# Kernel tuning notes

Hardware: AMD Instinct MI355X
Metric: run time of the kernel (lower is better)

Reference implementation:

```python
import jax, jax.numpy as jnp
import numpy as np

H = 1024      # hidden_dim
C = 151       # len(obj_classes)
E = 200       # embed_dim (GloVe)
DIN = 2048    # inputs_dim
T = 32        # timesteps
B = 128       # batch size (uniform packed lengths)


def setup_inputs() -> dict:
    key = jax.random.key(0)
    ks = jax.random.split(key, 8)
    sequence_tensor = jax.random.normal(ks[0], (T * B, DIN), dtype=jnp.float32) * 0.1
    labels = jax.random.randint(ks[1], (T * B,), 0, C).astype(jnp.int64)
    embed = jax.random.normal(ks[2], (C + 1, E), dtype=jnp.float32) * 0.1   # obj_embed.weight
    Wi = jax.random.normal(ks[3], (DIN + E, 6 * H), dtype=jnp.float32) * 0.02  # input_linearity
    bi = jnp.zeros((6 * H,), dtype=jnp.float32)
    Ws = jax.random.normal(ks[4], (H, 5 * H), dtype=jnp.float32) * 0.02        # state_linearity
    bs = jnp.zeros((5 * H,), dtype=jnp.float32)
    Wo = jax.random.normal(ks[5], (H, C), dtype=jnp.float32) * 0.02            # out_obj
    bo = jnp.zeros((C,), dtype=jnp.float32)
    return {"sequence_tensor": sequence_tensor, "labels": labels, "embed": embed,
            "Wi": Wi, "bi": bi, "Ws": Ws, "bs": bs, "Wo": Wo, "bo": bo,
            "batch_size": B}


def reference(sequence_tensor, embed, Wi, bi, Ws, bs, Wo, bo, labels, batch_size):
    b = int(batch_size)
    t = sequence_tensor.shape[0] // b
    x = sequence_tensor.reshape(t, b, -1)          # [T, B, DIN] packed timestep-major
    lab = labels.reshape(t, b)                     # [T, B]
    h0 = jnp.zeros((b, H), dtype=sequence_tensor.dtype)
    c0 = jnp.zeros((b, H), dtype=sequence_tensor.dtype)
    e0 = jnp.broadcast_to(embed[0], (b, E))        # 'start' embedding

    def step(carry, inp):
        h, c, pe = carry
        xt, lt = inp
        ti = jnp.concatenate([xt, pe], axis=1)     # [B, DIN+E]
        pi = ti @ Wi + bi                          # [B, 6H]
        ps = h @ Ws + bs                           # [B, 5H]

        def gate(k):
            return pi[:, k * H:(k + 1) * H] + ps[:, k * H:(k + 1) * H]

        i_g = jax.nn.sigmoid(gate(0))
        f_g = jax.nn.sigmoid(gate(1))
        m_i = jnp.tanh(gate(2))
        o_g = jax.nn.sigmoid(gate(3))
        c_new = i_g * m_i + f_g * c
        out = o_g * jnp.tanh(c_new)
        hw = jax.nn.sigmoid(gate(4))
        h_new = hw * out + (1.0 - hw) * pi[:, 5 * H:6 * H]  # highway

        pred = h_new @ Wo + bo                     # [B, C]
        nzp = jnp.argmax(pred[:, 1:], axis=1) + 1  # best non-bg class
        l2e = jnp.where(lt == 0, nzp.astype(lt.dtype), lt)
        pe_new = embed[l2e + 1]                    # feedback embedding
        return (h_new, c_new, pe_new), (pred, l2e)

    _, (dists, comms) = jax.lax.scan(step, (h0, c0, e0), (x, lab))
    return dists.reshape(t * b, C), comms.reshape(t * b)
```

## Files before the change

kernel.cpp:

```cpp
#include <hip/hip_runtime.h>
#include <math.h>

#define H    1024
#define C    151
#define E    200
#define DIN  2048
#define T    32
#define B    128
#define SIXH  (6*H)
#define FIVEH (5*H)
#define KTOT  DIN
#define NEMB  (C+1)
#define NWG   160
#define COLS  32

typedef _Float16 f16x8 __attribute__((ext_vector_type(8)));
typedef _Float16 f16x4 __attribute__((ext_vector_type(4)));
typedef float    f32x4 __attribute__((ext_vector_type(4)));

#define GLOAD_LDS16(g, l) __builtin_amdgcn_global_load_lds( \
    (const __attribute__((address_space(1))) unsigned int*)(g), \
    (__attribute__((address_space(3))) unsigned int*)(l), 16, 0, 0)

__device__ __forceinline__ void gbar(int* slots, int tid, int val) {
    __syncthreads();
    if (tid == 0)
        __hip_atomic_fetch_add(&slots[blockIdx.x * 16], 1,
                               __ATOMIC_ACQ_REL, __HIP_MEMORY_SCOPE_AGENT);
    int ok;
    do {
        int v = val;
        if (tid < NWG)
            v = __hip_atomic_load(&slots[tid * 16],
                                  __ATOMIC_RELAXED, __HIP_MEMORY_SCOPE_AGENT);
        ok = __syncthreads_and(v >= val);
        if (!ok) __builtin_amdgcn_s_sleep(1);
    } while (!ok);
    __builtin_amdgcn_fence(__ATOMIC_ACQUIRE, "agent");
}

__global__ void init_kernel(float* h, float* c, _Float16* hhi, _Float16* hlo,
                            int* eidx, int* bar) {
    int i = blockIdx.x * blockDim.x + threadIdx.x;
    if (i < B * H) {
        h[i] = 0.f; c[i] = 0.f;
        hhi[i] = (_Float16)0.f; hlo[i] = (_Float16)0.f;
    }
    if (i < B) eidx[i] = 0;
    if (i < NWG * 16) bar[i] = 0;
}

__global__ void cvt_x(const float* __restrict__ X, _Float16* __restrict__ hi,
                      _Float16* __restrict__ lo) {
    size_t i = ((size_t)blockIdx.x * 256 + threadIdx.x) * 4;
    float4 v = *(const float4*)(X + i);
    f16x4 h, l;
    h.x = (_Float16)v.x; l.x = (_Float16)(v.x - (float)h.x);
    h.y = (_Float16)v.y; l.y = (_Float16)(v.y - (float)h.y);
    h.z = (_Float16)v.z; l.z = (_Float16)(v.z - (float)h.z);
    h.w = (_Float16)v.w; l.w = (_Float16)(v.w - (float)h.w);
    *(f16x4*)(hi + i) = h;
    *(f16x4*)(lo + i) = l;
}

template<int KR, int NC>
__global__ void cvt_wT(const float* __restrict__ W, _Float16* __restrict__ hi,
                       _Float16* __restrict__ lo) {
    __shared__ float tile[32][33];
    int n0 = blockIdx.x * 32, k0 = blockIdx.y * 32;
    int tx = threadIdx.x & 31, ty = threadIdx.x >> 5;
    #pragma unroll
    for (int i = 0; i < 4; ++i) {
        int k = ty + i * 8;
        tile[k][tx] = W[(size_t)(k0 + k) * NC + n0 + tx];
    }
    __syncthreads();
    #pragma unroll
    for (int i = 0; i < 4; ++i) {
        int n = ty + i * 8;
        float v = tile[tx][n];
        _Float16 h = (_Float16)v;
        size_t o = (size_t)(n0 + n) * KR + k0 + tx;
        hi[o] = h;
        lo[o] = (_Float16)(v - (float)h);
    }
}

__global__ void cvt_woT(const float* __restrict__ Wo, float* __restrict__ WoT) {
    int k = blockIdx.x * 256 + threadIdx.x;
    for (int c = 0; c < C; ++c)
        WoT[(size_t)c * H + k] = Wo[(size_t)k * C + c];
}

__global__ void etab_kernel(const float* __restrict__ embed,
                            const float* __restrict__ Wi,
                            float* __restrict__ Etab) {
    int n = blockIdx.x * 256 + threadIdx.x;
    int k = blockIdx.y;
    const float* wp = Wi + (size_t)DIN * SIXH + n;
    const float* ep = embed + k * E;
    float acc = 0.f;
    #pragma unroll 8
    for (int e = 0; e < E; ++e)
        acc = fmaf(ep[e], wp[(size_t)e * SIXH], acc);
    Etab[(size_t)k * SIXH + n] = acc;
}

__global__ __launch_bounds__(256) void big_gemm_mfma(
    const _Float16* __restrict__ Ahi, const _Float16* __restrict__ Alo,
    const _Float16* __restrict__ Bhi, const _Float16* __restrict__ Blo,
    const float* __restrict__ bi, float* __restrict__ P)
{
    __shared__ __align__(16) _Float16 sAh[128 * 32];
    __shared__ __align__(16) _Float16 sAl[128 * 32];
    __shared__ __align__(16) _Float16 sBh[128 * 32];
    __shared__ __align__(16) _Float16 sBl[128 * 32];
    const int tid = threadIdx.x;
    const int n0 = blockIdx.x * 128;
    const int m0 = blockIdx.y * 128;
    const int lane = tid & 63, w = tid >> 6;
    const int wm = (w >> 1) * 64, wn = (w & 1) * 64;
    const int lr = lane & 15, lq = lane >> 4;

    f32x4 acc[4][4];
    #pragma unroll
    for (int i = 0; i < 4; ++i)
        #pragma unroll
        for (int j = 0; j < 4; ++j)
            acc[i][j] = (f32x4){0.f, 0.f, 0.f, 0.f};

    const int row0 = tid >> 2;
    const int kc = tid & 3;
    const int kcs = kc ^ ((row0 >> 1) & 3);
    const int sw = (lq ^ ((lr >> 1) & 3)) * 8;

    for (int k0 = 0; k0 < KTOT; k0 += 32) {
        #pragma unroll
        for (int i = 0; i < 2; ++i) {
            int row = row0 + i * 64;
            size_t ga = (size_t)(m0 + row) * KTOT + k0 + kcs * 8;
            size_t gb = (size_t)(n0 + row) * KTOT + k0 + kcs * 8;
            int loff = (i * 256 + tid) * 8;
            GLOAD_LDS16(Ahi + ga, sAh + loff);
            GLOAD_LDS16(Alo + ga, sAl + loff);
            GLOAD_LDS16(Bhi + gb, sBh + loff);
            GLOAD_LDS16(Blo + gb, sBl + loff);
        }
        __syncthreads();
        f16x8 ah[4], al[4], bh[4], bl[4];
        #pragma unroll
        for (int i = 0; i < 4; ++i) {
            ah[i] = *(const f16x8*)&sAh[(wm + i * 16 + lr) * 32 + sw];
            al[i] = *(const f16x8*)&sAl[(wm + i * 16 + lr) * 32 + sw];
            bh[i] = *(const f16x8*)&sBh[(wn + i * 16 + lr) * 32 + sw];
            bl[i] = *(const f16x8*)&sBl[(wn + i * 16 + lr) * 32 + sw];
        }
        #pragma unroll
        for (int i = 0; i < 4; ++i)
            #pragma unroll
            for (int j = 0; j < 4; ++j) {
                acc[i][j] = __builtin_amdgcn_mfma_f32_16x16x32_f16(ah[i], bh[j], acc[i][j], 0, 0, 0);
                acc[i][j] = __builtin_amdgcn_mfma_f32_16x16x32_f16(ah[i], bl[j], acc[i][j], 0, 0, 0);
                acc[i][j] = __builtin_amdgcn_mfma_f32_16x16x32_f16(al[i], bh[j], acc[i][j], 0, 0, 0);
            }
        __syncthreads();
    }
    #pragma unroll
    for (int i = 0; i < 4; ++i)
        #pragma unroll
        for (int j = 0; j < 4; ++j) {
            int gcol = n0 + wn + j * 16 + lr;
            float bv = bi[gcol];
            #pragma unroll
            for (int r = 0; r < 4; ++r) {
                int grow = m0 + wm + i * 16 + lq * 4 + r;
                P[(size_t)grow * SIXH + gcol] = acc[i][j][r] + bv;
            }
        }
}

__global__ __launch_bounds__(256, 1) void fused_loop(
    const float* __restrict__ P,
    const float* __restrict__ Etab,
    const float* __restrict__ bs,
    const _Float16* __restrict__ WsThi,
    const _Float16* __restrict__ WsTlo,
    _Float16* __restrict__ hhi,
    _Float16* __restrict__ hlo,
    float* __restrict__ ps,
    const float* __restrict__ WoT,
    const float* __restrict__ bo,
    const int* __restrict__ labels,
    float* __restrict__ dists,
    float* __restrict__ comms,
    int* bar)
{
    __shared__ __align__(16) _Float16 sBh[COLS * H];
    __shared__ __align__(16) _Float16 sBl[COLS * H];
    __shared__ __align__(16) float hs[H];
    __shared__ float vals[256];
    __shared__ int   idxs[256];
    __shared__ int   s_eidx;

    const int wg  = blockIdx.x;
    const int tid = threadIdx.x;
    const int n0  = wg * COLS;
    const int lane = tid & 63, w = tid >> 6;
    const int lr = lane & 15, lq = lane >> 4;

    for (int gi = tid; gi < COLS * (H / 8); gi += 256) {
        int col = gi >> 7;
        int kg  = gi & 127;
        int dst = (col * (H * 2) + kg * 16) ^ ((col & 7) << 4);
        *(f16x8*)((char*)sBh + dst) = *(const f16x8*)&WsThi[(size_t)(n0 + col) * H + kg * 8];
        *(f16x8*)((char*)sBl + dst) = *(const f16x8*)&WsTlo[(size_t)(n0 + col) * H + kg * 8];
    }

    float creg[4] = {0.f, 0.f, 0.f, 0.f};
    float bsr[4][5];
    if (wg < B) {
        #pragma unroll
        for (int jj = 0; jj < 4; ++jj)
            #pragma unroll
            for (int k = 0; k < 5; ++k)
                bsr[jj][k] = bs[k * H + jj * 256 + tid];
    }
    if (tid == 0) s_eidx = 0;
    __syncthreads();

    const int mrow0 = w * 32;
    int bval = 0;

    for (int t = 0; t < T; ++t) {
        int eidx_cur = s_eidx;

        f32x4 acc[2][2];
        #pragma unroll
        for (int i = 0; i < 2; ++i)
            #pragma unroll
            for (int j = 0; j < 2; ++j)
                acc[i][j] = (f32x4){0.f, 0.f, 0.f, 0.f};

        #pragma unroll 4
        for (int k0 = 0; k0 < H; k0 += 32) {
            f16x8 ah[2], al[2], bh[2], bl[2];
            #pragma unroll
            for (int i = 0; i < 2; ++i) {
                size_t ho = (size_t)(mrow0 + i * 16 + lr) * H + k0 + lq * 8;
                ah[i] = *(const f16x8*)&hhi[ho];
                al[i] = *(const f16x8*)&hlo[ho];
            }
            #pragma unroll
            for (int j = 0; j < 2; ++j) {
                int col = j * 16 + lr;
                int off = (col * (H * 2) + (k0 + lq * 8) * 2) ^ ((col & 7) << 4);
                bh[j] = *(const f16x8*)((const char*)sBh + off);
                bl[j] = *(const f16x8*)((const char*)sBl + off);
            }
            #pragma unroll
            for (int i = 0; i < 2; ++i)
                #pragma unroll
                for (int j = 0; j < 2; ++j) {
                    acc[i][j] = __builtin_amdgcn_mfma_f32_16x16x32_f16(ah[i], bh[j], acc[i][j], 0, 0, 0);
                    acc[i][j] = __builtin_amdgcn_mfma_f32_16x16x32_f16(ah[i], bl[j], acc[i][j], 0, 0, 0);
                    acc[i][j] = __builtin_amdgcn_mfma_f32_16x16x32_f16(al[i], bh[j], acc[i][j], 0, 0, 0);
                }
        }
        #pragma unroll
        for (int i = 0; i < 2; ++i)
            #pragma unroll
            for (int j = 0; j < 2; ++j)
                #pragma unroll
                for (int r = 0; r < 4; ++r)
                    ps[(size_t)(mrow0 + i * 16 + lq * 4 + r) * FIVEH + n0 + j * 16 + lr] = acc[i][j][r];

        float pf[4][6], pe[4][6];
        if (wg < B) {
            const float* prow = P + (size_t)(t * B + wg) * SIXH;
            const float* erow = Etab + (size_t)eidx_cur * SIXH;
            #pragma unroll
            for (int jj = 0; jj < 4; ++jj)
                #pragma unroll
                for (int k = 0; k < 6; ++k) {
                    pf[jj][k] = prow[k * H + jj * 256 + tid];
                    pe[jj][k] = erow[k * H + jj * 256 + tid];
                }
        }

        ++bval; gbar(bar, tid, bval);

        if (wg < B) {
            const int b = wg;
            const float* psr = ps + (size_t)b * FIVEH;
            #pragma unroll
            for (int jj = 0; jj < 4; ++jj) {
                int j = jj * 256 + tid;
                float gv[5];
                #pragma unroll
                for (int k = 0; k < 5; ++k)
                    gv[k] = pf[jj][k] + pe[jj][k] + psr[k * H + j] + bsr[jj][k];
                float pi5 = pf[jj][5] + pe[jj][5];
                float ig = 1.f / (1.f + expf(-gv[0]));
                float fg = 1.f / (1.f + expf(-gv[1]));
                float mi = tanhf(gv[2]);
                float og = 1.f / (1.f + expf(-gv[3]));
                float hw = 1.f / (1.f + expf(-gv[4]));
                float cn = ig * mi + fg * creg[jj];
                float out = og * tanhf(cn);
                float hn = hw * out + (1.f - hw) * pi5;
                creg[jj] = cn;
                hs[j] = hn;
                _Float16 hh = (_Float16)hn;
                hhi[(size_t)b * H + j] = hh;
                hlo[(size_t)b * H + j] = (_Float16)(hn - (float)hh);
            }
            __syncthreads();
            float predv = 0.f;
            if (tid < C) {
                const float* wp = WoT + (size_t)tid * H;
                float a0 = bo[tid], a1 = 0.f, a2 = 0.f, a3 = 0.f;
                #pragma unroll 4
                for (int k = 0; k < H; k += 4) {
                    float4 w4 = *(const float4*)&wp[k];
                    float4 h4 = *(const float4*)&hs[k];
                    a0 = fmaf(h4.x, w4.x, a0);
                    a1 = fmaf(h4.y, w4.y, a1);
                    a2 = fmaf(h4.z, w4.z, a2);
                    a3 = fmaf(h4.w, w4.w, a3);
                }
                predv = (a0 + a1) + (a2 + a3);
                dists[(size_t)(t * B + b) * C + tid] = predv;
            }
            vals[tid] = (tid >= 1 && tid < C) ? predv : -1e30f;
            idxs[tid] = tid;
            __syncthreads();
            for (int s = 128; s > 0; s >>= 1) {
                if (tid < s) {
                    float v2 = vals[tid + s];
                    int   i2 = idxs[tid + s];
                    if (v2 > vals[tid] || (v2 == vals[tid] && i2 < idxs[tid])) {
                        vals[tid] = v2;
                        idxs[tid] = i2;
                    }
                }
                __syncthreads();
            }
            if (tid == 0) {
                int nzp = idxs[0];
                int lt = labels[t * B + b];
                int comm = (lt == 0) ? nzp : lt;
                comms[t * B + b] = (float)comm;
                s_eidx = comm + 1;
            }
        }
        ++bval; gbar(bar, tid, bval);
    }
}

__global__ __launch_bounds__(256) void ps_mfma(
    const _Float16* __restrict__ Ahi, const _Float16* __restrict__ Alo,
    const _Float16* __restrict__ Bhi, const _Float16* __restrict__ Blo,
    float* __restrict__ ps)
{
    __shared__ __align__(16) _Float16 sAh[64 * 32];
    __shared__ __align__(16) _Float16 sAl[64 * 32];
    __shared__ __align__(16) _Float16 sBh[64 * 32];
    __shared__ __align__(16) _Float16 sBl[64 * 32];
    const int tid = threadIdx.x;
    const int n0 = blockIdx.x * 64;
    const int m0 = blockIdx.y * 64;
    const int lane = tid & 63, w = tid >> 6;
    const int wm = (w >> 1) * 32, wn = (w & 1) * 32;
    const int lr = lane & 15, lq = lane >> 4;

    f32x4 acc[2][2];
    #pragma unroll
    for (int i = 0; i < 2; ++i)
        #pragma unroll
        for (int j = 0; j < 2; ++j)
            acc[i][j] = (f32x4){0.f, 0.f, 0.f, 0.f};

    const int row = tid >> 2;
    const int kc = tid & 3;

    for (int k0 = 0; k0 < H; k0 += 32) {
        size_t ga = (size_t)(m0 + row) * H + k0 + kc * 8;
        size_t gb = (size_t)(n0 + row) * H + k0 + kc * 8;
        int loff = tid * 8;
        GLOAD_LDS16(Ahi + ga, sAh + loff);
        GLOAD_LDS16(Alo + ga, sAl + loff);
        GLOAD_LDS16(Bhi + gb, sBh + loff);
        GLOAD_LDS16(Blo + gb, sBl + loff);
        __syncthreads();
        f16x8 ah[2], al[2], bh[2], bl[2];
        #pragma unroll
        for (int i = 0; i < 2; ++i) {
            ah[i] = *(const f16x8*)&sAh[(wm + i * 16 + lr) * 32 + lq * 8];
            al[i] = *(const f16x8*)&sAl[(wm + i * 16 + lr) * 32 + lq * 8];
            bh[i] = *(const f16x8*)&sBh[(wn + i * 16 + lr) * 32 + lq * 8];
            bl[i] = *(const f16x8*)&sBl[(wn + i * 16 + lr) * 32 + lq * 8];
        }
        #pragma unroll
        for (int i = 0; i < 2; ++i)
            #pragma unroll
            for (int j = 0; j < 2; ++j) {
                acc[i][j] = __builtin_amdgcn_mfma_f32_16x16x32_f16(ah[i], bh[j], acc[i][j], 0, 0, 0);
                acc[i][j] = __builtin_amdgcn_mfma_f32_16x16x32_f16(ah[i], bl[j], acc[i][j], 0, 0, 0);
                acc[i][j] = __builtin_amdgcn_mfma_f32_16x16x32_f16(al[i], bh[j], acc[i][j], 0, 0, 0);
            }
        __syncthreads();
    }
    #pragma unroll
    for (int i = 0; i < 2; ++i)
        #pragma unroll
        for (int j = 0; j < 2; ++j) {
            int gcol = n0 + wn + j * 16 + lr;
            #pragma unroll
            for (int r = 0; r < 4; ++r) {
                int grow = m0 + wm + i * 16 + lq * 4 + r;
                ps[(size_t)grow * FIVEH + gcol] = acc[i][j][r];
            }
        }
}

__global__ void gate_kernel(const float* __restrict__ P,
                            const float* __restrict__ Etab,
                            const float* __restrict__ ps,
                            const float* __restrict__ bs,
                            const int* __restrict__ eidx,
                            float* __restrict__ h,
                            float* __restrict__ c,
                            _Float16* __restrict__ hhi,
                            _Float16* __restrict__ hlo,
                            int t) {
    int j = blockIdx.x * 256 + threadIdx.x;
    int b = blockIdx.y;
    const float* prow = P + (size_t)(t * B + b) * SIXH;
    const float* erow = Etab + (size_t)eidx[b] * SIXH;
    const float* psr  = ps + (size_t)b * FIVEH;
    float g[5];
    #pragma unroll
    for (int k = 0; k < 5; ++k) {
        int col = k * H + j;
        g[k] = prow[col] + erow[col] + psr[col] + bs[col];
    }
    float pi5 = prow[5 * H + j] + erow[5 * H + j];
    float ig = 1.f / (1.f + expf(-g[0]));
    float fg = 1.f / (1.f + expf(-g[1]));
    float mi = tanhf(g[2]);
    float og = 1.f / (1.f + expf(-g[3]));
    float hw = 1.f / (1.f + expf(-g[4]));
    float cv = c[b * H + j];
    float cn = ig * mi + fg * cv;
    float out = og * tanhf(cn);
    float hn = hw * out + (1.f - hw) * pi5;
    c[b * H + j] = cn;
    h[b * H + j] = hn;
    _Float16 hh = (_Float16)hn;
    hhi[b * H + j] = hh;
    hlo[b * H + j] = (_Float16)(hn - (float)hh);
}

__global__ void pred_kernel(const float* __restrict__ h,
                            const float* __restrict__ Wo,
                            const float* __restrict__ bo,
                            const int* __restrict__ labels,
                            float* __restrict__ dists,
                            float* __restrict__ comms,
                            int* __restrict__ eidx,
                            int t) {
    __shared__ float hsb[H];
    __shared__ float vals[256];
    __shared__ int   idxs[256];
    int tid = threadIdx.x;
    int b = blockIdx.x;
    for (int i = tid; i < H / 4; i += 256)
        *(float4*)&hsb[i * 4] = *(const float4*)&h[b * H + i * 4];
    __syncthreads();
    float pred = 0.f;
    if (tid < C) {
        pred = bo[tid];
        #pragma unroll 8
        for (int k = 0; k < H; ++k)
            pred = fmaf(hsb[k], Wo[k * C + tid], pred);
        dists[(size_t)(t * B + b) * C + tid] = pred;
    }
    vals[tid] = (tid >= 1 && tid < C) ? pred : -1e30f;
    idxs[tid] = tid;
    __syncthreads();
    for (int s = 128; s > 0; s >>= 1) {
        if (tid < s) {
            float v2 = vals[tid + s];
            int   i2 = idxs[tid + s];
            if (v2 > vals[tid] || (v2 == vals[tid] && i2 < idxs[tid])) {
                vals[tid] = v2;
                idxs[tid] = i2;
            }
        }
        __syncthreads();
    }
    if (tid == 0) {
        int nzp = idxs[0];
        int lt = labels[t * B + b];
        int comm = (lt == 0) ? nzp : lt;
        comms[t * B + b] = (float)comm;
        eidx[b] = comm + 1;
    }
}

extern "C" void kernel_launch(void* const* d_in, const int* in_sizes, int n_in,
                              void* d_out, int out_size, void* d_ws, size_t ws_size,
                              hipStream_t stream) {
    const float* X      = (const float*)d_in[0];
    const int*   labels = (const int*)  d_in[1];
    const float* embed  = (const float*)d_in[2];
    const float* Wi     = (const float*)d_in[3];
    const float* bi     = (const float*)d_in[4];
    const float* Ws     = (const float*)d_in[5];
    const float* bs     = (const float*)d_in[6];
    const float* Wo     = (const float*)d_in[7];
    const float* bo     = (const float*)d_in[8];

    char* w = (char*)d_ws;
    float* P      = (float*)w;              w += (size_t)T * B * SIXH * 4;
    float* Etab   = (float*)w;              w += (size_t)NEMB * SIXH * 4;
    float* ps     = (float*)w;              w += (size_t)B * FIVEH * 4;
    float* h      = (float*)w;              w += (size_t)B * H * 4;
    float* c      = (float*)w;              w += (size_t)B * H * 4;
    _Float16* hhi = (_Float16*)w;           w += (size_t)B * H * 2;
    _Float16* hlo = (_Float16*)w;           w += (size_t)B * H * 2;
    int* eidx     = (int*)w;                w += 512;
    int* bar      = (int*)w;                w += 16384;
    _Float16* Xhi = (_Float16*)w;           w += (size_t)T * B * KTOT * 2;
    _Float16* Xlo = (_Float16*)w;           w += (size_t)T * B * KTOT * 2;
    _Float16* WiThi = (_Float16*)w;         w += (size_t)SIXH * KTOT * 2;
    _Float16* WiTlo = (_Float16*)w;         w += (size_t)SIXH * KTOT * 2;
    _Float16* WsThi = (_Float16*)w;         w += (size_t)FIVEH * H * 2;
    _Float16* WsTlo = (_Float16*)w;         w += (size_t)FIVEH * H * 2;
    float* WoT    = (float*)Xhi;

    float* dists = (float*)d_out;
    float* comms = dists + (size_t)T * B * C;

    init_kernel<<<512, 256, 0, stream>>>(h, c, hhi, hlo, eidx, bar);
    cvt_x<<<(T * B * KTOT) / (256 * 4), 256, 0, stream>>>(X, Xhi, Xlo);
    cvt_wT<KTOT, SIXH><<<dim3(SIXH / 32, KTOT / 32), 256, 0, stream>>>(Wi, WiThi, WiTlo);
    cvt_wT<H, FIVEH><<<dim3(FIVEH / 32, H / 32), 256, 0, stream>>>(Ws, WsThi, WsTlo);
    etab_kernel<<<dim3(SIXH / 256, NEMB), 256, 0, stream>>>(embed, Wi, Etab);
    big_gemm_mfma<<<dim3(SIXH / 128, (T * B) / 128), 256, 0, stream>>>(Xhi, Xlo, WiThi, WiTlo, bi, P);
    cvt_woT<<<dim3(H / 256), 256, 0, stream>>>(Wo, WoT);

    void* args[] = {(void*)&P, (void*)&Etab, (void*)&bs, (void*)&WsThi, (void*)&WsTlo,
                    (void*)&hhi, (void*)&hlo, (void*)&ps, (void*)&WoT, (void*)&bo,
                    (void*)&labels, (void*)&dists, (void*)&comms, (void*)&bar};
    hipError_t err = hipLaunchCooperativeKernel((void*)fused_loop, dim3(NWG), dim3(256),
                                                args, 0, stream);
    if (err != hipSuccess) {
        for (int t = 0; t < T; ++t) {
            ps_mfma<<<dim3(FIVEH / 64, B / 64), 256, 0, stream>>>(hhi, hlo, WsThi, WsTlo, ps);
            gate_kernel<<<dim3(H / 256, B), 256, 0, stream>>>(P, Etab, ps, bs, eidx, h, c, hhi, hlo, t);
            pred_kernel<<<B, 256, 0, stream>>>(h, Wo, bo, labels, dists, comms, eidx, t);
        }
    }
}
```

Before: 2.434 ms.

## Centralize grid barrier via epoch flag and use wavefront-shuffle argmax

Replaces the all-to-all grid barrier, where every workgroup polled all 160 slots, with a master-based scheme. Workgroup 0 gathers the arrivals and publishes an epoch value, and the other workgroups spin on that single word. This cuts polling traffic on the atomics but adds an extra hop of latency through block 0. The shared-memory tree argmax with eight __syncthreads is replaced by a wavefront shuffle reduction plus a 4-way final pass, and the recurrent GEMM loop unroll goes from 4 to 8.

```diff
diff --git a/kernel.cpp b/kernel.cpp
--- a/kernel.cpp
+++ b/kernel.cpp
@@ -22,20 +22,31 @@
     (const __attribute__((address_space(1))) unsigned int*)(g), \
     (__attribute__((address_space(3))) unsigned int*)(l), 16, 0, 0)
 
-__device__ __forceinline__ void gbar(int* slots, int tid, int val) {
+__device__ __forceinline__ void gbar(int* slots, int* epoch, int tid, int val) {
     __syncthreads();
     if (tid == 0)
         __hip_atomic_fetch_add(&slots[blockIdx.x * 16], 1,
-                               __ATOMIC_ACQ_REL, __HIP_MEMORY_SCOPE_AGENT);
-    int ok;
-    do {
-        int v = val;
-        if (tid < NWG)
-            v = __hip_atomic_load(&slots[tid * 16],
-                                  __ATOMIC_RELAXED, __HIP_MEMORY_SCOPE_AGENT);
-        ok = __syncthreads_and(v >= val);
-        if (!ok) __builtin_amdgcn_s_sleep(1);
-    } while (!ok);
+                               __ATOMIC_RELEASE, __HIP_MEMORY_SCOPE_AGENT);
+    if (blockIdx.x == 0) {
+        int ok;
+        do {
+            int v = val;
+            if (tid < NWG)
+                v = __hip_atomic_load(&slots[tid * 16],
+                                      __ATOMIC_RELAXED, __HIP_MEMORY_SCOPE_AGENT);
+            ok = __syncthreads_and(v >= val);
+            if (!ok) __builtin_amdgcn_s_sleep(1);
+        } while (!ok);
+        if (tid == 0)
+            __hip_atomic_store(epoch, val, __ATOMIC_RELEASE, __HIP_MEMORY_SCOPE_AGENT);
+    } else {
+        int ok;
+        do {
+            int v = __hip_atomic_load(epoch, __ATOMIC_RELAXED, __HIP_MEMORY_SCOPE_AGENT);
+            ok = __syncthreads_and(v >= val);
+            if (!ok) __builtin_amdgcn_s_sleep(1);
+        } while (!ok);
+    }
     __builtin_amdgcn_fence(__ATOMIC_ACQUIRE, "agent");
 }
 
@@ -47,7 +58,7 @@
         hhi[i] = (_Float16)0.f; hlo[i] = (_Float16)0.f;
     }
     if (i < B) eidx[i] = 0;
-    if (i < NWG * 16) bar[i] = 0;
+    if (i < NWG * 16 + 16) bar[i] = 0;
 }
 
 __global__ void cvt_x(const float* __restrict__ X, _Float16* __restrict__ hi,
@@ -198,8 +209,8 @@
     __shared__ __align__(16) _Float16 sBh[COLS * H];
     __shared__ __align__(16) _Float16 sBl[COLS * H];
     __shared__ __align__(16) float hs[H];
-    __shared__ float vals[256];
-    __shared__ int   idxs[256];
+    __shared__ float vals[8];
+    __shared__ int   idxs[8];
     __shared__ int   s_eidx;
 
     const int wg  = blockIdx.x;
@@ -207,6 +218,7 @@
     const int n0  = wg * COLS;
     const int lane = tid & 63, w = tid >> 6;
     const int lr = lane & 15, lq = lane >> 4;
+    int* epoch = bar + NWG * 16;
 
     for (int gi = tid; gi < COLS * (H / 8); gi += 256) {
         int col = gi >> 7;
@@ -241,7 +253,7 @@
             for (int j = 0; j < 2; ++j)
                 acc[i][j] = (f32x4){0.f, 0.f, 0.f, 0.f};
 
-        #pragma unroll 4
+        #pragma unroll 8
         for (int k0 = 0; k0 < H; k0 += 32) {
             f16x8 ah[2], al[2], bh[2], bl[2];
             #pragma unroll
@@ -287,7 +299,7 @@
                 }
         }
 
-        ++bval; gbar(bar, tid, bval);
+        ++bval; gbar(bar, epoch, tid, bval);
 
         if (wg < B) {
             const int b = wg;
@@ -331,29 +343,30 @@
                 predv = (a0 + a1) + (a2 + a3);
                 dists[(size_t)(t * B + b) * C + tid] = predv;
             }
-            vals[tid] = (tid >= 1 && tid < C) ? predv : -1e30f;
-            idxs[tid] = tid;
+            float av = (tid >= 1 && tid < C) ? predv : -1e30f;
+            int   ai = tid;
+            #pragma unroll
+            for (int s = 32; s > 0; s >>= 1) {
+                float v2 = __shfl_down(av, s, 64);
+                int   i2 = __shfl_down(ai, s, 64);
+                if (v2 > av || (v2 == av && i2 < ai)) { av = v2; ai = i2; }
+            }
+            if (lane == 0) { vals[w] = av; idxs[w] = ai; }
             __syncthreads();
-            for (int s = 128; s > 0; s >>= 1) {
-                if (tid < s) {
-                    float v2 = vals[tid + s];
-                    int   i2 = idxs[tid + s];
-                    if (v2 > vals[tid] || (v2 == vals[tid] && i2 < idxs[tid])) {
-                        vals[tid] = v2;
-                        idxs[tid] = i2;
+            if (tid == 0) {
+                float bv2 = vals[0]; int bi2 = idxs[0];
+                #pragma unroll
+                for (int k = 1; k < 4; ++k)
+                    if (vals[k] > bv2 || (vals[k] == bv2 && idxs[k] < bi2)) {
+                        bv2 = vals[k]; bi2 = idxs[k];
                     }
-                }
-                __syncthreads();
-            }
-            if (tid == 0) {
-                int nzp = idxs[0];
                 int lt = labels[t * B + b];
-                int comm = (lt == 0) ? nzp : lt;
+                int comm = (lt == 0) ? bi2 : lt;
                 comms[t * B + b] = (float)comm;
                 s_eidx = comm + 1;
             }
         }
-        ++bval; gbar(bar, tid, bval);
+        ++bval; gbar(bar, epoch, tid, bval);
     }
 }
 
```

Result: no change. 2.459 ms (+1.1%).
